# Performance work log

Hardware: AMD Instinct MI355X
Metric: run time of the kernel (lower is better)

## Reference

```python
import jax, jax.numpy as jnp
import numpy as np

IH, IW = 32, 32
N = IH * IW            # tokens
C = 256                # inp == oup
HEADS, DH = 8, 32
INNER = HEADS * DH     # 256
HID = 2 * C            # 512
EPS = 1e-5
SCALE = DH ** -0.5


def _relative_index():
    ci = np.stack(np.meshgrid(np.arange(IH), np.arange(IW), indexing='ij')).reshape(2, -1)
    rel = ci[:, :, None] - ci[:, None, :]          # [2, n, n]
    rel[0] += IH - 1
    rel[1] += IW - 1
    rel[0] *= 2 * IW - 1
    return (rel[0] + rel[1]).astype(np.int32).reshape(-1)  # [n*n]


def setup_inputs() -> dict:
    key = jax.random.key(0)
    ks = jax.random.split(key, 12)
    B = 16
    s = lambda k, shape, scale=0.02: jax.random.normal(k, shape, jnp.float32) * scale
    return {
        'x': jax.random.normal(ks[0], (B, C, IH, IW), jnp.float32),
        'rel_index': jnp.asarray(_relative_index()),
        'ln1_g': jnp.ones((C,), jnp.float32),
        'ln1_b': jnp.zeros((C,), jnp.float32),
        'Wqkv': s(ks[1], (C, 3 * INNER)),
        'table': s(ks[2], ((2 * IH - 1) * (2 * IW - 1), HEADS)),
        'Wo': s(ks[3], (INNER, C)),
        'bo': jnp.zeros((C,), jnp.float32),
        'ln2_g': jnp.ones((C,), jnp.float32),
        'ln2_b': jnp.zeros((C,), jnp.float32),
        'W1': s(ks[4], (C, HID)),
        'b1': jnp.zeros((HID,), jnp.float32),
        'W2': s(ks[5], (HID, C)),
        'b2': jnp.zeros((C,), jnp.float32),
    }


def _ln(t, g, b):
    mu = t.mean(-1, keepdims=True)
    var = ((t - mu) ** 2).mean(-1, keepdims=True)
    return (t - mu) * jax.lax.rsqrt(var + EPS) * g + b


def reference(x, rel_index, ln1_g, ln1_b, Wqkv, table, Wo, bo, ln2_g, ln2_b, W1, b1, W2, b2):
    B = x.shape[0]
    t = jnp.transpose(x.reshape(B, C, N), (0, 2, 1))  # [B, n, C]
    # --- attention sub-block (PreNorm) ---
    h = _ln(t, ln1_g, ln1_b)
    qkv = h @ Wqkv                                    # [B, n, 3*inner]
    q, k, v = jnp.split(qkv, 3, axis=-1)
    tohd = lambda u: jnp.transpose(u.reshape(B, N, HEADS, DH), (0, 2, 1, 3))  # bhnd
    q, k, v = tohd(q), tohd(k), tohd(v)
    dots = jnp.einsum('bhnd,bhmd->bhnm', q, k) * SCALE
    bias = table[rel_index].reshape(N, N, HEADS).transpose(2, 0, 1)[None]  # [1,h,n,n]
    attn = jax.nn.softmax(dots + bias, axis=-1)
    out = jnp.einsum('bhnm,bhmd->bhnd', attn, v)
    out = jnp.transpose(out, (0, 2, 1, 3)).reshape(B, N, INNER)
    out = out @ Wo + bo
    t = t + out
    # --- feed-forward sub-block (PreNorm) ---
    h = _ln(t, ln2_g, ln2_b)
    h = jax.nn.gelu(h @ W1 + b1, approximate=False)
    h = h @ W2 + b2
    t = t + h
    return jnp.transpose(t, (0, 2, 1)).reshape(B, C, IH, IW)
```

## Files before the change

### kernel.cpp

```cpp
#include <hip/hip_runtime.h>
#include <hip/hip_bf16.h>
#include <math.h>

typedef __bf16 bfx4 __attribute__((ext_vector_type(4)));
typedef __bf16 bfx8 __attribute__((ext_vector_type(8)));
typedef float  f32x4 __attribute__((ext_vector_type(4)));

#define BATCH 16
#define NTOK  1024
#define CDIM  256
#define NHEAD 8
#define DHEAD 32
#define QKVD  768
#define INNER 256
#define SCALE 0.17677669529663687f
#define LOG2E 1.4426950408889634f

#if __has_builtin(__builtin_amdgcn_exp2f)
#define EXP2(x) __builtin_amdgcn_exp2f(x)
#else
#define EXP2(x) exp2f(x)
#endif

__launch_bounds__(256)
__global__ void txln_kernel(const float* __restrict__ x, const float* __restrict__ g,
                            const float* __restrict__ bb, __bf16* __restrict__ tb,
                            __bf16* __restrict__ hln) {
  __shared__ float tile[256][65];
  const int b = blockIdx.z, n0 = blockIdx.x * 64;
  const int tt = threadIdx.x;
  const float* src = x + (size_t)b * CDIM * NTOK;
  const int rc = tt >> 4, nc = (tt & 15) * 4;
  #pragma unroll
  for (int i = 0; i < 16; ++i) {
    int c = rc + i * 16;
    *(float4*)&tile[c][nc] = *(const float4*)&src[(size_t)c * NTOK + n0 + nc];
  }
  __syncthreads();
  const int n = tt >> 2, c0 = (tt & 3) * 64;
  float vals[64];
  float s = 0.f, s2 = 0.f;
  #pragma unroll
  for (int j = 0; j < 64; ++j) {
    float v = tile[c0 + j][n];
    vals[j] = v; s += v; s2 += v * v;
  }
  s  += __shfl_xor(s, 1);  s  += __shfl_xor(s, 2);
  s2 += __shfl_xor(s2, 1); s2 += __shfl_xor(s2, 2);
  float mu = s * 0.00390625f;
  float var = s2 * 0.00390625f - mu * mu;
  float rs = rsqrtf(var + 1e-5f);
  size_t row = ((size_t)b * NTOK + n0 + n) * CDIM;
  #pragma unroll
  for (int j = 0; j < 64; j += 4) {
    const float4 gg = *(const float4*)&g[c0 + j];
    const float4 bv = *(const float4*)&bb[c0 + j];
    bfx4 tv;
    tv[0] = (__bf16)vals[j];     tv[1] = (__bf16)vals[j + 1];
    tv[2] = (__bf16)vals[j + 2]; tv[3] = (__bf16)vals[j + 3];
    *(bfx4*)&tb[row + c0 + j] = tv;
    bfx4 o;
    o[0] = (__bf16)((vals[j]     - mu) * rs * gg.x + bv.x);
    o[1] = (__bf16)((vals[j + 1] - mu) * rs * gg.y + bv.y);
    o[2] = (__bf16)((vals[j + 2] - mu) * rs * gg.z + bv.z);
    o[3] = (__bf16)((vals[j + 3] - mu) * rs * gg.w + bv.w);
    *(bfx4*)&hln[row + c0 + j] = o;
  }
}

__launch_bounds__(256)
__global__ void ln_kernel(const __bf16* __restrict__ in, const float* __restrict__ g,
                          const float* __restrict__ bb, __bf16* __restrict__ out) {
  int row  = blockIdx.x * 4 + (threadIdx.x >> 6);
  int lane = threadIdx.x & 63;
  const bfx4 vb = *(const bfx4*)(in + (size_t)row * 256 + lane * 4);
  float4 v;
  v.x = (float)vb[0]; v.y = (float)vb[1]; v.z = (float)vb[2]; v.w = (float)vb[3];
  float s  = v.x + v.y + v.z + v.w;
  float s2 = v.x * v.x + v.y * v.y + v.z * v.z + v.w * v.w;
  #pragma unroll
  for (int o = 32; o; o >>= 1) { s += __shfl_xor(s, o); s2 += __shfl_xor(s2, o); }
  float mu  = s * 0.00390625f;
  float var = s2 * 0.00390625f - mu * mu;
  float rs  = rsqrtf(var + 1e-5f);
  const float4 gg = ((const float4*)g)[lane];
  const float4 bv = ((const float4*)bb)[lane];
  bfx4 o4;
  o4[0] = (__bf16)((v.x - mu) * rs * gg.x + bv.x);
  o4[1] = (__bf16)((v.y - mu) * rs * gg.y + bv.y);
  o4[2] = (__bf16)((v.z - mu) * rs * gg.z + bv.z);
  o4[3] = (__bf16)((v.w - mu) * rs * gg.w + bv.w);
  *(bfx4*)(out + (size_t)row * 256 + lane * 4) = o4;
}

__launch_bounds__(256)
__global__ void prep_kernel(const float* __restrict__ Wqkv, const float* __restrict__ Wo,
                            const float* __restrict__ W1, const float* __restrict__ W2,
                            __bf16* __restrict__ Wqkvt, __bf16* __restrict__ Wot,
                            __bf16* __restrict__ W1t, __bf16* __restrict__ W2t,
                            const float* __restrict__ table, __bf16* __restrict__ biasB) {
  if (blockIdx.x < 2048) {
    int idx = blockIdx.x * 256 + threadIdx.x;
    const float* W; __bf16* Wt; int lk, Nn, off;
    if (idx < 196608)      { W = Wqkv; Wt = Wqkvt; lk = 8; Nn = 768; off = idx; }
    else if (idx < 262144) { W = Wo;   Wt = Wot;   lk = 8; Nn = 256; off = idx - 196608; }
    else if (idx < 393216) { W = W1;   Wt = W1t;   lk = 8; Nn = 512; off = idx - 262144; }
    else                   { W = W2;   Wt = W2t;   lk = 9; Nn = 256; off = idx - 393216; }
    int n = off >> lk, k = off & ((1 << lk) - 1);
    Wt[off] = (__bf16)W[(size_t)k * Nn + n];
  } else {
    int idx = (blockIdx.x - 2048) * 256 + threadIdx.x;
    int k8 = (idx & 127) * 8, q = (idx >> 7) & 1023, h = idx >> 17;
    int qi = q >> 5, qj = q & 31;
    bfx8 o;
    #pragma unroll
    for (int j = 0; j < 8; ++j) {
      int k = k8 + j, ki = k >> 5, kj = k & 31;
      int r = (qi - ki + 31) * 63 + (qj - kj + 31);
      o[j] = (__bf16)(table[r * 8 + h] * LOG2E);
    }
    *(bfx8*)&biasB[((size_t)idx) * 8] = o;
  }
}

template <int EPI>
__launch_bounds__(256)
__global__ void gemm128_kernel(const __bf16* __restrict__ A, const __bf16* __restrict__ Bt,
                               const float* __restrict__ bias,
                               const __bf16* __restrict__ residb,
                               void* __restrict__ outp, __bf16* __restrict__ vTout,
                               int Nn, int K) {
  __shared__ char smem[36864];
  __bf16 (*As)[72] = (__bf16(*)[72])smem;
  __bf16 (*Bs)[72] = (__bf16(*)[72])(smem + 18432);
  const int t = threadIdx.x, lane = t & 63, w = t >> 6;
  const int m0 = blockIdx.x * 128, n0 = blockIdx.y * 128;
  const int wr = w >> 1, wc = w & 1;
  const int lr = lane & 15, kb = (lane >> 4) * 4;
  int srow[4], sp0[4], sp1[4];
  #pragma unroll
  for (int i = 0; i < 4; ++i) {
    int cid = i * 256 + t, kb8 = (cid & 7) * 8;
    srow[i] = cid >> 3;
    int b0 = kb8, b1 = kb8 + 4;
    sp0[i] = (b0 & 32) + ((b0 & 12) << 1) + (((b0 >> 4) & 1) << 2) + (b0 & 3);
    sp1[i] = (b1 & 32) + ((b1 & 12) << 1) + (((b1 >> 4) & 1) << 2) + (b1 & 3);
  }
  f32x4 acc[4][4] = {};
  bfx8 ra[4], rb[4];
  auto gload = [&](int k0) {
    #pragma unroll
    for (int i = 0; i < 4; ++i) {
      int kc8 = ((i * 256 + t) & 7) * 8;
      ra[i] = *(const bfx8*)&A[(size_t)(m0 + srow[i]) * K + k0 + kc8];
      rb[i] = *(const bfx8*)&Bt[(size_t)(n0 + srow[i]) * K + k0 + kc8];
    }
  };
  gload(0);
  for (int k0 = 0; k0 < K; k0 += 64) {
    __syncthreads();
    #pragma unroll
    for (int i = 0; i < 4; ++i) {
      *(bfx4*)&As[srow[i]][sp0[i]] = __builtin_shufflevector(ra[i], ra[i], 0, 1, 2, 3);
      *(bfx4*)&As[srow[i]][sp1[i]] = __builtin_shufflevector(ra[i], ra[i], 4, 5, 6, 7);
      *(bfx4*)&Bs[srow[i]][sp0[i]] = __builtin_shufflevector(rb[i], rb[i], 0, 1, 2, 3);
      *(bfx4*)&Bs[srow[i]][sp1[i]] = __builtin_shufflevector(rb[i], rb[i], 4, 5, 6, 7);
    }
    __syncthreads();
    if (k0 + 64 < K) gload(k0 + 64);
    #pragma unroll
    for (int ks = 0; ks < 2; ++ks) {
      bfx8 af[4], bf[4];
      #pragma unroll
      for (int mi = 0; mi < 4; ++mi)
        af[mi] = *(const bfx8*)&As[wr * 64 + mi * 16 + lr][ks * 32 + kb * 2];
      #pragma unroll
      for (int ni = 0; ni < 4; ++ni)
        bf[ni] = *(const bfx8*)&Bs[wc * 64 + ni * 16 + lr][ks * 32 + kb * 2];
      #pragma unroll
      for (int mi = 0; mi < 4; ++mi)
        #pragma unroll
        for (int ni = 0; ni < 4; ++ni)
          acc[mi][ni] = __builtin_amdgcn_mfma_f32_16x16x32_bf16(af[mi], bf[ni],
                                                                acc[mi][ni], 0, 0, 0);
    }
  }
  if (EPI == 4) {
    float* Ty = (float*)smem;
    const int bb_ = m0 >> 10, tok0 = m0 & 1023;
    float* obase = (float*)outp + (size_t)bb_ * CDIM * NTOK + tok0;
    #pragma unroll
    for (int h2 = 0; h2 < 2; ++h2) {
      __syncthreads();
      if (wc == h2) {
        #pragma unroll
        for (int ni = 0; ni < 4; ++ni) {
          int ch = ni * 16 + lr;
          float bn = bias[n0 + h2 * 64 + ch];
          #pragma unroll
          for (int mi = 0; mi < 4; ++mi) {
            int tk = wr * 64 + mi * 16 + kb;
            float4 v4;
            #pragma unroll
            for (int r = 0; r < 4; ++r)
              ((float*)&v4)[r] = acc[mi][ni][r] + bn +
                  (float)residb[(size_t)(m0 + tk + r) * Nn + n0 + h2 * 64 + ch];
            *(float4*)&Ty[ch * 132 + tk] = v4;
          }
        }
      }
      __syncthreads();
      int ch = t >> 2, sc = t & 3;
      #pragma unroll
      for (int j = 0; j < 8; ++j) {
        int c4 = sc + j * 4;
        *(float4*)&obase[(size_t)(n0 + h2 * 64 + ch) * NTOK + c4 * 4] =
            *(const float4*)&Ty[ch * 132 + c4 * 4];
      }
    }
    return;
  }
  if (EPI == 0 && vTout != nullptr && n0 >= 512) {
    #pragma unroll
    for (int mi = 0; mi < 4; ++mi)
      #pragma unroll
      for (int ni = 0; ni < 4; ++ni) {
        int n = n0 + wc * 64 + ni * 16 + lr;
        int cp = n - 512, hh = cp >> 5, dd = cp & 31;
        int m = m0 + wr * 64 + mi * 16 + kb;
        int bb_ = m >> 10, tok = m & 1023;
        bfx4 o;
        o[0] = (__bf16)acc[mi][ni][0]; o[1] = (__bf16)acc[mi][ni][1];
        o[2] = (__bf16)acc[mi][ni][2]; o[3] = (__bf16)acc[mi][ni][3];
        *(bfx4*)&vTout[(((size_t)bb_ * NHEAD + hh) * DHEAD + dd) * NTOK + tok] = o;
      }
    return;
  }
  #pragma unroll
  for (int mi = 0; mi < 4; ++mi)
    #pragma unroll
    for (int ni = 0; ni < 4; ++ni)
      #pragma unroll
      for (int r = 0; r < 4; ++r) {
        int m = m0 + wr * 64 + mi * 16 + kb + r;
        int n = n0 + wc * 64 + ni * 16 + lr;
        float v = acc[mi][ni][r];
        if (EPI == 0) {
          ((__bf16*)outp)[(size_t)m * Nn + n] = (__bf16)v;
        } else if (EPI == 1) {
          v += bias[n] + (float)residb[(size_t)m * Nn + n];
          ((__bf16*)outp)[(size_t)m * Nn + n] = (__bf16)v;
        } else if (EPI == 2) {
          v += bias[n];
          v = 0.5f * v * (1.0f + erff(v * 0.70710678118f));
          ((__bf16*)outp)[(size_t)m * Nn + n] = (__bf16)v;
        }
      }
}

__launch_bounds__(512)
__global__ void attn_kernel(const __bf16* __restrict__ qkv, const __bf16* __restrict__ vT,
                            const __bf16* __restrict__ biasB, __bf16* __restrict__ outb) {
  __shared__ __bf16 Ks[64][40];
  __shared__ __bf16 Vs[32][72];
  __shared__ __bf16 Bls[256][72];
  const int q0 = blockIdx.x * 256, h = blockIdx.y, b = blockIdx.z;
  const int t = threadIdx.x, lane = t & 63, w = t >> 6;
  const int lr = lane & 15, kb = (lane >> 4) * 4;
  const size_t qbase = (size_t)b * NTOK * QKVD;
  const float qsc = SCALE * LOG2E;
  bfx8 qf[2];
  #pragma unroll
  for (int tq = 0; tq < 2; ++tq) {
    const __bf16* qp = &qkv[qbase + (size_t)(q0 + 32 * w + 16 * tq + lr) * QKVD + h * DHEAD];
    bfx4 lo = *(const bfx4*)&qp[kb];
    bfx4 hi = *(const bfx4*)&qp[kb + 16];
    #pragma unroll
    for (int j = 0; j < 4; ++j) {
      qf[tq][j]     = (__bf16)((float)lo[j] * qsc);
      qf[tq][j + 4] = (__bf16)((float)hi[j] * qsc);
    }
  }
  float l_run[2] = {0.f, 0.f};
  f32x4 oacc[2][2] = {};
  const int st_ = t & 255;
  const int krow = st_ >> 2, kc8 = (st_ & 3) * 8;
  const int vrow = st_ >> 3, vc8 = (st_ & 7) * 8;
  const __bf16* kvptr = (t < 256)
      ? &qkv[qbase + (size_t)krow * QKVD + INNER + h * DHEAD + kc8]
      : &vT[(((size_t)b * NHEAD + h) * DHEAD + vrow) * NTOK + vc8];
  const __bf16* bbase = &biasB[((size_t)h * NTOK + q0) * NTOK];
  bfx8 rkv, rbias[4];
  auto issue = [&](int k0) {
    rkv = (t < 256) ? *(const bfx8*)&kvptr[(size_t)k0 * QKVD]
                    : *(const bfx8*)&kvptr[k0];
    #pragma unroll
    for (int j = 0; j < 4; ++j) {
      int lin = j * 512 + t;
      int br = lin >> 3, bc8 = (lin & 7) * 8;
      rbias[j] = *(const bfx8*)&bbase[(size_t)br * NTOK + k0 + bc8];
    }
  };
  issue(0);
  for (int kt = 0; kt < 16; ++kt) {
    __syncthreads();
    if (t < 256) *(bfx8*)&Ks[krow][kc8] = rkv;
    else         *(bfx8*)&Vs[vrow][vc8] = rkv;
    #pragma unroll
    for (int j = 0; j < 4; ++j) {
      int lin = j * 512 + t;
      int br = lin >> 3, bc8 = (lin & 7) * 8;
      *(bfx8*)&Bls[br][bc8] = rbias[j];
    }
    __syncthreads();
    if (kt < 15) issue((kt + 1) * 64);
    bfx8 kf[4], vfr[4];
    #pragma unroll
    for (int f = 0; f < 4; ++f) {
      bfx4 klo = *(const bfx4*)&Ks[16 * f + lr][kb];
      bfx4 khi = *(const bfx4*)&Ks[16 * f + lr][kb + 16];
      kf[f] = __builtin_shufflevector(klo, khi, 0, 1, 2, 3, 4, 5, 6, 7);
    }
    #pragma unroll
    for (int s = 0; s < 2; ++s)
      #pragma unroll
      for (int df = 0; df < 2; ++df) {
        bfx4 vlo = *(const bfx4*)&Vs[16 * df + lr][s * 32 + kb];
        bfx4 vhi = *(const bfx4*)&Vs[16 * df + lr][s * 32 + kb + 16];
        vfr[s * 2 + df] = __builtin_shufflevector(vlo, vhi, 0, 1, 2, 3, 4, 5, 6, 7);
      }
    #pragma unroll
    for (int tq = 0; tq < 2; ++tq) {
      const int qrow_l = 32 * w + 16 * tq + lr;
      f32x4 st[4];
      #pragma unroll
      for (int f = 0; f < 4; ++f) {
        bfx4 bv = *(const bfx4*)&Bls[qrow_l][16 * f + kb];
        f32x4 c;
        c[0] = (float)bv[0]; c[1] = (float)bv[1];
        c[2] = (float)bv[2]; c[3] = (float)bv[3];
        st[f] = __builtin_amdgcn_mfma_f32_16x16x32_bf16(kf[f], qf[tq], c, 0, 0, 0);
      }
      float p[4][4], tsum = 0.f;
      #pragma unroll
      for (int f = 0; f < 4; ++f)
        #pragma unroll
        for (int r = 0; r < 4; ++r) {
          float e = EXP2(st[f][r]);
          p[f][r] = e;
          tsum += e;
        }
      l_run[tq] += tsum;
      bfx8 pa0, pa1;
      #pragma unroll
      for (int r = 0; r < 4; ++r) {
        pa0[r] = (__bf16)p[0][r];  pa0[r + 4] = (__bf16)p[1][r];
        pa1[r] = (__bf16)p[2][r];  pa1[r + 4] = (__bf16)p[3][r];
      }
      #pragma unroll
      for (int s = 0; s < 2; ++s) {
        bfx8 pa = s ? pa1 : pa0;
        #pragma unroll
        for (int df = 0; df < 2; ++df)
          oacc[tq][df] = __builtin_amdgcn_mfma_f32_16x16x32_bf16(pa, vfr[s * 2 + df],
                                                                 oacc[tq][df], 0, 0, 0);
      }
    }
  }
  #pragma unroll
  for (int tq = 0; tq < 2; ++tq) {
    float l = l_run[tq];
    l += __shfl_xor(l, 16);
    l += __shfl_xor(l, 32);
    float il[4];
    #pragma unroll
    for (int r = 0; r < 4; ++r) il[r] = 1.f / __shfl(l, kb + r);
    #pragma unroll
    for (int r = 0; r < 4; ++r) {
      size_t rowoff = (size_t)b * NTOK * CDIM +
                      (size_t)(q0 + 32 * w + 16 * tq + kb + r) * CDIM + h * DHEAD;
      outb[rowoff + lr]      = (__bf16)(oacc[tq][0][r] * il[r]);
      outb[rowoff + 16 + lr] = (__bf16)(oacc[tq][1][r] * il[r]);
    }
  }
}

extern "C" void kernel_launch(void* const* d_in, const int* in_sizes, int n_in,
                              void* d_out, int out_size, void* d_ws, size_t ws_size,
                              hipStream_t stream) {
  const float* x     = (const float*)d_in[0];
  const float* ln1_g = (const float*)d_in[2];
  const float* ln1_b = (const float*)d_in[3];
  const float* Wqkv  = (const float*)d_in[4];
  const float* table = (const float*)d_in[5];
  const float* Wo    = (const float*)d_in[6];
  const float* bo    = (const float*)d_in[7];
  const float* ln2_g = (const float*)d_in[8];
  const float* ln2_b = (const float*)d_in[9];
  const float* W1    = (const float*)d_in[10];
  const float* b1    = (const float*)d_in[11];
  const float* W2    = (const float*)d_in[12];
  const float* b2    = (const float*)d_in[13];

  char* ws = (char*)d_ws;
  __bf16* t_bf  = (__bf16*)(ws + 0);
  __bf16* t2_bf = (__bf16*)(ws + 8388608);
  __bf16* qkv   = (__bf16*)(ws + 33554432);
  __bf16* hln   = (__bf16*)(ws + 58720256);
  __bf16* aout  = (__bf16*)(ws + 67108864);
  __bf16* hid   = (__bf16*)(ws + 75497472);
  __bf16* vT    = (__bf16*)(ws + 75497472);
  __bf16* biasB = (__bf16*)(ws + 92274688);
  __bf16* Wqkvt = (__bf16*)(ws + 109051904);
  __bf16* Wot   = (__bf16*)(ws + 109445120);
  __bf16* W1t   = (__bf16*)(ws + 109576192);
  __bf16* W2t   = (__bf16*)(ws + 109838336);
  if (ws_size < 110100480) return;

  prep_kernel<<<6144, 256, 0, stream>>>(Wqkv, Wo, W1, W2, Wqkvt, Wot, W1t, W2t,
                                        table, biasB);
  txln_kernel<<<dim3(16, 1, 16), 256, 0, stream>>>(x, ln1_g, ln1_b, t_bf, hln);
  gemm128_kernel<0><<<dim3(128, 6), 256, 0, stream>>>(hln, Wqkvt, nullptr, nullptr, qkv, vT, 768, 256);
  attn_kernel<<<dim3(4, 8, 16), 512, 0, stream>>>(qkv, vT, biasB, aout);
  gemm128_kernel<1><<<dim3(128, 2), 256, 0, stream>>>(aout, Wot, bo, t_bf, t2_bf, nullptr, 256, 256);
  ln_kernel<<<4096, 256, 0, stream>>>(t2_bf, ln2_g, ln2_b, hln);
  gemm128_kernel<2><<<dim3(128, 4), 256, 0, stream>>>(hln, W1t, b1, nullptr, hid, nullptr, 512, 256);
  gemm128_kernel<4><<<dim3(128, 2), 256, 0, stream>>>(hid, W2t, b2, t2_bf, d_out, nullptr, 256, 512);
}
```

Baseline: 131.5 us.

## Fuse Wo projection GEMM with residual add and second LayerNorm

Replaces the Wo GEMM plus separate LayerNorm kernel with one kernel. Each block computes a full 64-row by 256-column tile, adds bias and residual, reduces row statistics across waves through shared memory, and writes both t2 and the normalized hln. This removes one launch and a full read of t2 from global memory. The cost is a grid of 256 blocks with smaller M tiles and no double-buffered shared memory, so the GEMM itself may run less efficiently.

```diff
diff --git a/kernel.cpp b/kernel.cpp
--- a/kernel.cpp
+++ b/kernel.cpp
@@ -66,31 +66,6 @@
     o[3] = (__bf16)((vals[j + 3] - mu) * rs * gg.w + bv.w);
     *(bfx4*)&hln[row + c0 + j] = o;
   }
-}
-
-__launch_bounds__(256)
-__global__ void ln_kernel(const __bf16* __restrict__ in, const float* __restrict__ g,
-                          const float* __restrict__ bb, __bf16* __restrict__ out) {
-  int row  = blockIdx.x * 4 + (threadIdx.x >> 6);
-  int lane = threadIdx.x & 63;
-  const bfx4 vb = *(const bfx4*)(in + (size_t)row * 256 + lane * 4);
-  float4 v;
-  v.x = (float)vb[0]; v.y = (float)vb[1]; v.z = (float)vb[2]; v.w = (float)vb[3];
-  float s  = v.x + v.y + v.z + v.w;
-  float s2 = v.x * v.x + v.y * v.y + v.z * v.z + v.w * v.w;
-  #pragma unroll
-  for (int o = 32; o; o >>= 1) { s += __shfl_xor(s, o); s2 += __shfl_xor(s2, o); }
-  float mu  = s * 0.00390625f;
-  float var = s2 * 0.00390625f - mu * mu;
-  float rs  = rsqrtf(var + 1e-5f);
-  const float4 gg = ((const float4*)g)[lane];
-  const float4 bv = ((const float4*)bb)[lane];
-  bfx4 o4;
-  o4[0] = (__bf16)((v.x - mu) * rs * gg.x + bv.x);
-  o4[1] = (__bf16)((v.y - mu) * rs * gg.y + bv.y);
-  o4[2] = (__bf16)((v.z - mu) * rs * gg.z + bv.z);
-  o4[3] = (__bf16)((v.w - mu) * rs * gg.w + bv.w);
-  *(bfx4*)(out + (size_t)row * 256 + lane * 4) = o4;
 }
 
 __launch_bounds__(256)
@@ -247,15 +222,149 @@
         float v = acc[mi][ni][r];
         if (EPI == 0) {
           ((__bf16*)outp)[(size_t)m * Nn + n] = (__bf16)v;
-        } else if (EPI == 1) {
-          v += bias[n] + (float)residb[(size_t)m * Nn + n];
-          ((__bf16*)outp)[(size_t)m * Nn + n] = (__bf16)v;
         } else if (EPI == 2) {
           v += bias[n];
           v = 0.5f * v * (1.0f + erff(v * 0.70710678118f));
           ((__bf16*)outp)[(size_t)m * Nn + n] = (__bf16)v;
         }
       }
+}
+
+__launch_bounds__(512)
+__global__ void gemmWoLn_kernel(const __bf16* __restrict__ A, const __bf16* __restrict__ Bt,
+                                const float* __restrict__ bias,
+                                const __bf16* __restrict__ residb,
+                                const float* __restrict__ g2, const float* __restrict__ b2v,
+                                __bf16* __restrict__ t2, __bf16* __restrict__ hln) {
+  __shared__ char smem[46080];
+  __bf16 (*As)[72] = (__bf16(*)[72])smem;
+  __bf16 (*Bs)[72] = (__bf16(*)[72])(smem + 9216);
+  const int t = threadIdx.x, lane = t & 63, w = t >> 6;
+  const int m0 = blockIdx.x * 64;
+  const int wr = w >> 2, wc = w & 3;
+  const int lr = lane & 15, kb = (lane >> 4) * 4;
+  const int K = 256;
+  const int arow = t >> 3, ac8 = (t & 7) * 8;
+  int ap0, ap1;
+  {
+    int b0 = ac8, b1 = ac8 + 4;
+    ap0 = (b0 & 32) + ((b0 & 12) << 1) + (((b0 >> 4) & 1) << 2) + (b0 & 3);
+    ap1 = (b1 & 32) + ((b1 & 12) << 1) + (((b1 >> 4) & 1) << 2) + (b1 & 3);
+  }
+  int brow[4], bp0[4], bp1[4], bc8[4];
+  #pragma unroll
+  for (int j = 0; j < 4; ++j) {
+    int cid = j * 512 + t;
+    brow[j] = cid >> 3;
+    bc8[j] = (cid & 7) * 8;
+    int b0 = bc8[j], b1 = bc8[j] + 4;
+    bp0[j] = (b0 & 32) + ((b0 & 12) << 1) + (((b0 >> 4) & 1) << 2) + (b0 & 3);
+    bp1[j] = (b1 & 32) + ((b1 & 12) << 1) + (((b1 >> 4) & 1) << 2) + (b1 & 3);
+  }
+  f32x4 acc[2][4] = {};
+  bfx8 ra, rb[4];
+  auto gload = [&](int k0) {
+    ra = *(const bfx8*)&A[(size_t)(m0 + arow) * K + k0 + ac8];
+    #pragma unroll
+    for (int j = 0; j < 4; ++j)
+      rb[j] = *(const bfx8*)&Bt[(size_t)brow[j] * K + k0 + bc8[j]];
+  };
+  gload(0);
+  for (int k0 = 0; k0 < K; k0 += 64) {
+    __syncthreads();
+    *(bfx4*)&As[arow][ap0] = __builtin_shufflevector(ra, ra, 0, 1, 2, 3);
+    *(bfx4*)&As[arow][ap1] = __builtin_shufflevector(ra, ra, 4, 5, 6, 7);
+    #pragma unroll
+    for (int j = 0; j < 4; ++j) {
+      *(bfx4*)&Bs[brow[j]][bp0[j]] = __builtin_shufflevector(rb[j], rb[j], 0, 1, 2, 3);
+      *(bfx4*)&Bs[brow[j]][bp1[j]] = __builtin_shufflevector(rb[j], rb[j], 4, 5, 6, 7);
+    }
+    __syncthreads();
+    if (k0 + 64 < K) gload(k0 + 64);
+    #pragma unroll
+    for (int ks = 0; ks < 2; ++ks) {
+      bfx8 af[2], bf[4];
+      #pragma unroll
+      for (int mi = 0; mi < 2; ++mi)
+        af[mi] = *(const bfx8*)&As[wr * 32 + mi * 16 + lr][ks * 32 + kb * 2];
+      #pragma unroll
+      for (int ni = 0; ni < 4; ++ni)
+        bf[ni] = *(const bfx8*)&Bs[wc * 64 + ni * 16 + lr][ks * 32 + kb * 2];
+      #pragma unroll
+      for (int mi = 0; mi < 2; ++mi)
+        #pragma unroll
+        for (int ni = 0; ni < 4; ++ni)
+          acc[mi][ni] = __builtin_amdgcn_mfma_f32_16x16x32_bf16(af[mi], bf[ni],
+                                                                acc[mi][ni], 0, 0, 0);
+    }
+  }
+  float colg[4], colb[4];
+  #pragma unroll
+  for (int ni = 0; ni < 4; ++ni) {
+    int colq = wc * 64 + ni * 16 + lr;
+    float bn = bias[colq];
+    colg[ni] = g2[colq];
+    colb[ni] = b2v[colq];
+    #pragma unroll
+    for (int mi = 0; mi < 2; ++mi)
+      #pragma unroll
+      for (int r = 0; r < 4; ++r) {
+        int m = m0 + wr * 32 + mi * 16 + kb + r;
+        acc[mi][ni][r] += bn + (float)residb[(size_t)m * CDIM + colq];
+      }
+  }
+  float ps[2][4], pq[2][4];
+  #pragma unroll
+  for (int mi = 0; mi < 2; ++mi)
+    #pragma unroll
+    for (int r = 0; r < 4; ++r) {
+      float s = 0.f, q = 0.f;
+      #pragma unroll
+      for (int ni = 0; ni < 4; ++ni) {
+        float v = acc[mi][ni][r];
+        s += v; q += v * v;
+      }
+      #pragma unroll
+      for (int o = 1; o < 16; o <<= 1) { s += __shfl_xor(s, o); q += __shfl_xor(q, o); }
+      ps[mi][r] = s; pq[mi][r] = q;
+    }
+  __syncthreads();
+  float* red = (float*)smem;
+  if (lr == 0) {
+    #pragma unroll
+    for (int mi = 0; mi < 2; ++mi)
+      #pragma unroll
+      for (int r = 0; r < 4; ++r) {
+        int rl = wr * 32 + mi * 16 + kb + r;
+        red[rl * 8 + wc] = ps[mi][r];
+        red[rl * 8 + 4 + wc] = pq[mi][r];
+      }
+  }
+  __syncthreads();
+  if (t < 64) {
+    float s = red[t * 8] + red[t * 8 + 1] + red[t * 8 + 2] + red[t * 8 + 3];
+    float q = red[t * 8 + 4] + red[t * 8 + 5] + red[t * 8 + 6] + red[t * 8 + 7];
+    float mu = s * 0.00390625f;
+    float var = q * 0.00390625f - mu * mu;
+    red[t * 8] = mu;
+    red[t * 8 + 1] = rsqrtf(var + 1e-5f);
+  }
+  __syncthreads();
+  #pragma unroll
+  for (int mi = 0; mi < 2; ++mi)
+    #pragma unroll
+    for (int r = 0; r < 4; ++r) {
+      int rl = wr * 32 + mi * 16 + kb + r;
+      float mu = red[rl * 8], rs = red[rl * 8 + 1];
+      size_t rowoff = (size_t)(m0 + rl) * CDIM;
+      #pragma unroll
+      for (int ni = 0; ni < 4; ++ni) {
+        int colq = wc * 64 + ni * 16 + lr;
+        float v = acc[mi][ni][r];
+        t2[rowoff + colq] = (__bf16)v;
+        hln[rowoff + colq] = (__bf16)((v - mu) * rs * colg[ni] + colb[ni]);
+      }
+    }
 }
 
 __launch_bounds__(512)
@@ -422,8 +531,7 @@
   txln_kernel<<<dim3(16, 1, 16), 256, 0, stream>>>(x, ln1_g, ln1_b, t_bf, hln);
   gemm128_kernel<0><<<dim3(128, 6), 256, 0, stream>>>(hln, Wqkvt, nullptr, nullptr, qkv, vT, 768, 256);
   attn_kernel<<<dim3(4, 8, 16), 512, 0, stream>>>(qkv, vT, biasB, aout);
-  gemm128_kernel<1><<<dim3(128, 2), 256, 0, stream>>>(aout, Wot, bo, t_bf, t2_bf, nullptr, 256, 256);
-  ln_kernel<<<4096, 256, 0, stream>>>(t2_bf, ln2_g, ln2_b, hln);
+  gemmWoLn_kernel<<<256, 512, 0, stream>>>(aout, Wot, bo, t_bf, ln2_g, ln2_b, t2_bf, hln);
   gemm128_kernel<2><<<dim3(128, 4), 256, 0, stream>>>(hln, W1t, b1, nullptr, hid, nullptr, 512, 256);
   gemm128_kernel<4><<<dim3(128, 2), 256, 0, stream>>>(hid, W2t, b2, t2_bf, d_out, nullptr, 256, 512);
 }
```

Measured after the change: 131.0 us, median of 2. Within noise of the previous version (-0.4%).
